# Optimization experiments

Hardware: AMD Instinct MI355X
Metric: run time of the kernel (lower is better)

Reference implementation:

```python
import jax, jax.numpy as jnp
import numpy as np

N_LAYERS = 2
D_MODEL = 768
D_INNER = 1536
D_STATE = 16
D_CONV = 4
DT_RANK = 48
VOCAB = 50257
EPS = 1e-5


def _rms(x, w):
    return x * jax.lax.rsqrt(jnp.mean(x * x, axis=-1, keepdims=True) + EPS) * w


def _mixer(x, in_w, cw, cb, xp_w, dt_w, dt_b, a_log, d_skip, out_w):
    b, l, _ = x.shape
    xz = x @ in_w.T                                  # (b,l,2*d_in)
    u, z = jnp.split(xz, 2, axis=-1)                 # each (b,l,d_in)
    # causal depthwise conv1d
    uc = jax.lax.conv_general_dilated(
        u.transpose(0, 2, 1), cw[:, None, :], (1,), [(D_CONV - 1, 0)],
        feature_group_count=D_INNER, dimension_numbers=("NCH", "OIH", "NCH"))
    u = jax.nn.silu((uc + cb[:, None]).transpose(0, 2, 1))
    x_dbl = u @ xp_w.T                               # (b,l,dt_rank+2n)
    dt, B, C = jnp.split(x_dbl, [DT_RANK, DT_RANK + D_STATE], axis=-1)
    delta = jax.nn.softplus(dt @ dt_w.T + dt_b)      # (b,l,d_in)
    A = -jnp.exp(a_log)                              # (d_in,n)
    dA = jnp.exp(delta[..., None] * A)               # (b,l,d_in,n)
    dBu = delta[..., None] * B[:, :, None, :] * u[..., None]

    def step(h, inp):
        dA_t, dBu_t, C_t = inp
        h = dA_t * h + dBu_t
        return h, jnp.einsum("bdn,bn->bd", h, C_t)

    h0 = jnp.zeros((b, D_INNER, D_STATE), x.dtype)
    _, ys = jax.lax.scan(step, h0, (dA.transpose(1, 0, 2, 3),
                                    dBu.transpose(1, 0, 2, 3),
                                    C.transpose(1, 0, 2)))
    y = ys.transpose(1, 0, 2) + u * d_skip           # (b,l,d_in)
    y = y * jax.nn.silu(z)
    return y @ out_w.T


def setup_inputs() -> dict:
    key = jax.random.key(0)
    ks = jax.random.split(key, 12)
    std = 0.02
    emb = jax.random.normal(ks[0], (VOCAB, D_MODEL), jnp.float32) * std
    emb = emb.at[0].set(0.0)  # padding_idx=0
    tokens = jax.random.randint(ks[1], (2, 1024), 0, VOCAB)
    a_log = jnp.tile(jnp.log(jnp.arange(1, D_STATE + 1, dtype=jnp.float32)),
                     (N_LAYERS, D_INNER, 1))
    return {
        "tokens": tokens,
        "emb": emb,
        "norm_w": jnp.ones((N_LAYERS, D_MODEL), jnp.float32),
        "in_proj_w": jax.random.normal(ks[2], (N_LAYERS, 2 * D_INNER, D_MODEL), jnp.float32) * std,
        "conv_w": jax.random.normal(ks[3], (N_LAYERS, D_INNER, D_CONV), jnp.float32) * 0.1,
        "conv_b": jnp.zeros((N_LAYERS, D_INNER), jnp.float32),
        "x_proj_w": jax.random.normal(ks[4], (N_LAYERS, DT_RANK + 2 * D_STATE, D_INNER), jnp.float32) * std,
        "dt_proj_w": jax.random.normal(ks[5], (N_LAYERS, D_INNER, DT_RANK), jnp.float32) * (DT_RANK ** -0.5),
        "dt_proj_b": jax.random.uniform(ks[6], (N_LAYERS, D_INNER), jnp.float32, -4.6, -2.0),
        "A_log": a_log,
        "D": jnp.ones((N_LAYERS, D_INNER), jnp.float32),
        "out_proj_w": jax.random.normal(ks[7], (N_LAYERS, D_MODEL, D_INNER), jnp.float32) * (std / np.sqrt(2 * N_LAYERS)),
        "normf_w": jnp.ones((D_MODEL,), jnp.float32),
        "lm_head_w": jax.random.normal(ks[8], (VOCAB, D_MODEL), jnp.float32) * std,
    }


def reference(tokens, emb, norm_w, in_proj_w, conv_w, conv_b, x_proj_w,
              dt_proj_w, dt_proj_b, A_log, D, out_proj_w, normf_w, lm_head_w):
    x = emb[tokens]                                  # (b,l,d_model)
    for i in range(N_LAYERS):
        x = x + _mixer(_rms(x, norm_w[i]), in_proj_w[i], conv_w[i], conv_b[i],
                       x_proj_w[i], dt_proj_w[i], dt_proj_b[i], A_log[i],
                       D[i], out_proj_w[i])
    x = _rms(x, normf_w)
    return x @ lm_head_w.T                           # (b,l,vocab)
```

## Files before the change

### kernel.cpp

```cpp
#include <hip/hip_runtime.h>
#include <hip/hip_bf16.h>
#include <math.h>

#define DM 768
#define DI 1536
#define DSN 16
#define NB 2
#define SL 1024
#define MROWS 2048
#define VOC 50257
#define VOCP 50304
#define EPSR 1e-5f

typedef __attribute__((ext_vector_type(8))) short short8;
typedef __attribute__((ext_vector_type(4))) float f32x4;
typedef __attribute__((ext_vector_type(4))) unsigned short us4;
typedef unsigned short u16;

__device__ inline u16 f2bf(float f) {
    unsigned u = __builtin_bit_cast(unsigned, f);
    u += 0x7FFFu + ((u >> 16) & 1u);
    return (u16)(u >> 16);
}

__global__ void k_embed(const int* __restrict__ tok, const float* __restrict__ emb,
                        float* __restrict__ x) {
    int r = blockIdx.x;
    int t = tok[r];
    const float* src = emb + (size_t)t * DM;
    float* dst = x + (size_t)r * DM;
    for (int i = threadIdx.x; i < DM; i += 256) dst[i] = src[i];
}

__global__ __launch_bounds__(256)
void k_rmsnorm_bf16(const float* __restrict__ x, const float* __restrict__ w,
                    u16* __restrict__ out) {
    int r = blockIdx.x;
    const float* row = x + (size_t)r * DM;
    int c0 = threadIdx.x * 3;
    float v[3]; float ss = 0.f;
#pragma unroll
    for (int i = 0; i < 3; ++i) { v[i] = row[c0 + i]; ss += v[i] * v[i]; }
#pragma unroll
    for (int o = 32; o > 0; o >>= 1) ss += __shfl_down(ss, o);
    __shared__ float s[4];
    int lane = threadIdx.x & 63, wv = threadIdx.x >> 6;
    if (lane == 0) s[wv] = ss;
    __syncthreads();
    float sc = rsqrtf((s[0] + s[1] + s[2] + s[3]) / (float)DM + EPSR);
#pragma unroll
    for (int i = 0; i < 3; ++i)
        out[(size_t)r * DM + c0 + i] = f2bf(v[i] * sc * w[c0 + i]);
}

__global__ void k_cvt_pad4(const float* __restrict__ src, u16* __restrict__ dst,
                           int sr, int sc, int sld, int dc, long total4) {
    long i4 = (long)blockIdx.x * 256 + threadIdx.x;
    if (i4 >= total4) return;
    long i = i4 * 4;
    int r = (int)(i / dc), c0 = (int)(i % dc);
    us4 o;
#pragma unroll
    for (int e = 0; e < 4; ++e) {
        int c = c0 + e;
        float v = (r < sr && c < sc) ? src[(size_t)r * sld + c] : 0.f;
        o[e] = f2bf(v);
    }
    *(us4*)&dst[i] = o;
}

__global__ void k_conv_silu(const float* __restrict__ xz, const float* __restrict__ cw,
                            const float* __restrict__ cb, float* __restrict__ uc,
                            u16* __restrict__ ucb) {
    int d = blockIdx.x * 256 + threadIdx.x;
    int r = blockIdx.y;
    int l = r & (SL - 1);
    float acc = cb[d];
#pragma unroll
    for (int j = 0; j < 4; ++j) {
        int ls = l - 3 + j;
        if (ls >= 0) acc += xz[(size_t)(r - 3 + j) * (2 * DI) + d] * cw[d * 4 + j];
    }
    float s = acc / (1.f + __expf(-acc));
    uc[(size_t)r * DI + d] = s;
    ucb[(size_t)r * DI + d] = f2bf(s);
}

__global__ void k_softplus(const float* __restrict__ in, const float* __restrict__ b,
                           float* __restrict__ out) {
    int i = blockIdx.x * 256 + threadIdx.x;
    int d = i % DI;
    float v = in[i] + b[d];
    out[i] = (v > 20.f) ? v : log1pf(__expf(v));
}

__global__ __launch_bounds__(512)
void k_scan2(const float* __restrict__ delta, const float* __restrict__ uc,
             const float* __restrict__ xdbl, const float* __restrict__ xz,
             const float* __restrict__ alog, const float* __restrict__ Dp,
             u16* __restrict__ ybf) {
    __shared__ float ds2[8][16][20], us2[8][16][20], bn2[8][16][20], cn2[8][16][20];
    __shared__ float Sm[8][16][16], Pm[8][16][16];
    int b  = blockIdx.x / 96;
    int d0 = (blockIdx.x % 96) * 16;
    int tid = threadIdx.x, w = tid >> 6, lane = tid & 63;
    int ch = lane >> 2, nq = lane & 3;
    int d = d0 + ch;
    float A[4];
#pragma unroll
    for (int k = 0; k < 4; ++k) A[k] = -__expf(alog[d * DSN + nq + 4 * k]);
    int tb = w * 128;

    float h[4] = {0.f, 0.f, 0.f, 0.f};
    float sdl = 0.f;
    for (int t0 = 0; t0 < 128; t0 += 16) {
        int row0 = b * SL + tb + t0;
#pragma unroll
        for (int i = 0; i < 4; ++i) {
            int lin = i * 64 + lane, tt = lin >> 4, cc = lin & 15;
            size_t row = (size_t)(row0 + tt);
            ds2[w][cc][tt] = delta[row * DI + d0 + cc];
            us2[w][cc][tt] = uc[row * DI + d0 + cc];
            bn2[w][cc][tt] = xdbl[row * 128 + 48 + cc];
        }
#pragma unroll
        for (int g4 = 0; g4 < 4; ++g4) {
            f32x4 dl = *(const f32x4*)&ds2[w][ch][g4 * 4];
            f32x4 uv = *(const f32x4*)&us2[w][ch][g4 * 4];
            f32x4 bv[4];
#pragma unroll
            for (int k = 0; k < 4; ++k) bv[k] = *(const f32x4*)&bn2[w][nq + 4 * k][g4 * 4];
#pragma unroll
            for (int s = 0; s < 4; ++s) {
                float du = dl[s] * uv[s];
                sdl += dl[s];
#pragma unroll
                for (int k = 0; k < 4; ++k) {
                    float dA = __expf(dl[s] * A[k]);
                    h[k] = h[k] * dA + du * bv[k][s];
                }
            }
        }
    }
#pragma unroll
    for (int k = 0; k < 4; ++k) {
        Sm[w][ch][nq + 4 * k] = h[k];
        Pm[w][ch][nq + 4 * k] = __expf(A[k] * sdl);
    }
    __syncthreads();
    if (tid < 256) {
        int c2 = tid >> 4, n2 = tid & 15;
        float H = 0.f;
#pragma unroll
        for (int g = 0; g < 8; ++g) {
            float hi = H;
            H = Pm[g][c2][n2] * H + Sm[g][c2][n2];
            Sm[g][c2][n2] = hi;
        }
    }
    __syncthreads();
    float Dv = Dp[d];
#pragma unroll
    for (int k = 0; k < 4; ++k) h[k] = Sm[w][ch][nq + 4 * k];
    for (int t0 = 0; t0 < 128; t0 += 16) {
        int row0 = b * SL + tb + t0;
#pragma unroll
        for (int i = 0; i < 4; ++i) {
            int lin = i * 64 + lane, tt = lin >> 4, cc = lin & 15;
            size_t row = (size_t)(row0 + tt);
            ds2[w][cc][tt] = delta[row * DI + d0 + cc];
            us2[w][cc][tt] = uc[row * DI + d0 + cc];
            bn2[w][cc][tt] = xdbl[row * 128 + 48 + cc];
            cn2[w][cc][tt] = xdbl[row * 128 + 64 + cc];
        }
#pragma unroll
        for (int g4 = 0; g4 < 4; ++g4) {
            f32x4 dl = *(const f32x4*)&ds2[w][ch][g4 * 4];
            f32x4 uv = *(const f32x4*)&us2[w][ch][g4 * 4];
            f32x4 bv[4], cv[4];
#pragma unroll
            for (int k = 0; k < 4; ++k) {
                bv[k] = *(const f32x4*)&bn2[w][nq + 4 * k][g4 * 4];
                cv[k] = *(const f32x4*)&cn2[w][nq + 4 * k][g4 * 4];
            }
#pragma unroll
            for (int s = 0; s < 4; ++s) {
                float du = dl[s] * uv[s];
                float p = 0.f;
#pragma unroll
                for (int k = 0; k < 4; ++k) {
                    float dA = __expf(dl[s] * A[k]);
                    h[k] = h[k] * dA + du * bv[k][s];
                    p += h[k] * cv[k][s];
                }
                p += __shfl_xor(p, 1);
                p += __shfl_xor(p, 2);
                if (nq == 0) {
                    size_t row = (size_t)(row0 + g4 * 4 + s);
                    float z = xz[row * (2 * DI) + DI + d];
                    float y = p + uv[s] * Dv;
                    y *= z / (1.f + __expf(-z));
                    ybf[row * DI + d] = f2bf(y);
                }
            }
        }
    }
}

template <bool ADD_RES, bool NGUARD>
__global__ __launch_bounds__(256)
void k_gemm_bt(const u16* __restrict__ A, const u16* __restrict__ W,
               float* __restrict__ C, const float* __restrict__ RES,
               int K, int ldc, int nmax, int nTm) {
    __shared__ u16 Al[128 * 32];
    __shared__ u16 Wl[128 * 32];
    int nwg = gridDim.x;
    int qc = nwg >> 3, rc = nwg & 7;
    int xcd = blockIdx.x & 7, j = blockIdx.x >> 3;
    int wg = (xcd < rc ? xcd * (qc + 1) : rc * (qc + 1) + (xcd - rc) * qc) + j;
    int m0 = (wg % nTm) * 128, n0 = (wg / nTm) * 128;

    int tid = threadIdx.x, wave = tid >> 6, lane = tid & 63;
    int wm = wave >> 1, wn = wave & 1;
    f32x4 acc[4][4] = {};
    const int rS = (lane >> 2);
    const int kS = (((lane & 3) ^ ((lane >> 3) & 3)) * 8);
    const int kofs = (((lane >> 4) ^ ((lane >> 1) & 3)) * 8);
    const int fr = lane & 15;

    for (int k0 = 0; k0 < K; k0 += 32) {
#pragma unroll
        for (int i = 0; i < 2; ++i) {
            int rowA = m0 + wave * 32 + i * 16 + rS;
            const u16* ga = A + (size_t)rowA * K + k0 + kS;
            __builtin_amdgcn_global_load_lds(
                (const __attribute__((address_space(1))) void*)ga,
                (__attribute__((address_space(3))) void*)(&Al[wave * 1024 + i * 512]),
                16, 0, 0);
            int rowW = n0 + wave * 32 + i * 16 + rS;
            const u16* gw = W + (size_t)rowW * K + k0 + kS;
            __builtin_amdgcn_global_load_lds(
                (const __attribute__((address_space(1))) void*)gw,
                (__attribute__((address_space(3))) void*)(&Wl[wave * 1024 + i * 512]),
                16, 0, 0);
        }
        __syncthreads();
        short8 af[4], bfr[4];
#pragma unroll
        for (int f = 0; f < 4; ++f) {
            af[f]  = *(const short8*)&Al[(wm * 64 + f * 16 + fr) * 32 + kofs];
            bfr[f] = *(const short8*)&Wl[(wn * 64 + f * 16 + fr) * 32 + kofs];
        }
#pragma unroll
        for (int i = 0; i < 4; ++i)
#pragma unroll
            for (int jj = 0; jj < 4; ++jj)
                acc[i][jj] = __builtin_amdgcn_mfma_f32_16x16x32_bf16(af[i], bfr[jj], acc[i][jj], 0, 0, 0);
        __syncthreads();
    }
    int r4 = (lane >> 4) * 4;
#pragma unroll
    for (int i = 0; i < 4; ++i)
#pragma unroll
        for (int jj = 0; jj < 4; ++jj) {
            int col = n0 + wn * 64 + jj * 16 + fr;
            if (NGUARD && col >= nmax) continue;
#pragma unroll
            for (int rr = 0; rr < 4; ++rr) {
                int row = m0 + wm * 64 + i * 16 + r4 + rr;
                size_t off = (size_t)row * ldc + col;
                float v = acc[i][jj][rr];
                if (ADD_RES) v += RES[off];
                C[off] = v;
            }
        }
}

extern "C" void kernel_launch(void* const* d_in, const int* in_sizes, int n_in,
                              void* d_out, int out_size, void* d_ws, size_t ws_size,
                              hipStream_t stream) {
    (void)in_sizes; (void)n_in; (void)out_size;
    const int*   tok   = (const int*)d_in[0];
    const float* emb   = (const float*)d_in[1];
    const float* normw = (const float*)d_in[2];
    const float* inw   = (const float*)d_in[3];
    const float* cw    = (const float*)d_in[4];
    const float* cb    = (const float*)d_in[5];
    const float* xpw   = (const float*)d_in[6];
    const float* dtw   = (const float*)d_in[7];
    const float* dtb   = (const float*)d_in[8];
    const float* alog  = (const float*)d_in[9];
    const float* Dp    = (const float*)d_in[10];
    const float* outw  = (const float*)d_in[11];
    const float* normf = (const float*)d_in[12];
    const float* lmw   = (const float*)d_in[13];
    float* out = (float*)d_out;

    char* p = (char*)d_ws;
    auto alloc = [&](size_t bytes) { char* r = p; p += (bytes + 255) & ~(size_t)255; return r; };
    float* x     = (float*)alloc((size_t)MROWS * DM * 4);
    u16*   xnb   = (u16*)  alloc((size_t)MROWS * DM * 2);
    float* xz    = (float*)alloc((size_t)MROWS * 2 * DI * 4);
    float* uc    = (float*)alloc((size_t)MROWS * DI * 4);
    u16*   ucb   = (u16*)  alloc((size_t)MROWS * DI * 2);
    float* xdbl  = (float*)alloc((size_t)MROWS * 128 * 4);
    u16*   xdblb = (u16*)  alloc((size_t)MROWS * 64 * 2);
    float* dtraw = (float*)alloc((size_t)MROWS * DI * 4);
    float* delta = (float*)alloc((size_t)MROWS * DI * 4);
    u16*   ybf   = (u16*)  alloc((size_t)MROWS * DI * 2);
    u16*   winb  = (u16*)  alloc((size_t)(2 * DI) * DM * 2);
    u16*   wxpb  = (u16*)  alloc((size_t)128 * DI * 2);
    u16*   wdtb  = (u16*)  alloc((size_t)DI * 64 * 2);
    u16*   woutb = (u16*)  alloc((size_t)DM * DI * 2);
    u16*   wlmb  = (u16*)  alloc((size_t)VOCP * DM * 2);
    if ((size_t)(p - (char*)d_ws) > ws_size) return;

    {
        long t4 = (long)VOCP * DM / 4;
        k_cvt_pad4<<<dim3((unsigned)((t4 + 255) / 256)), 256, 0, stream>>>(
            lmw, wlmb, VOC, DM, DM, DM, t4);
    }

    k_embed<<<MROWS, 256, 0, stream>>>(tok, emb, x);

    for (int i = 0; i < NB; ++i) {
        k_rmsnorm_bf16<<<MROWS, 256, 0, stream>>>(x, normw + i * DM, xnb);

        { long t4 = (long)(2 * DI) * DM / 4;
          k_cvt_pad4<<<dim3((unsigned)((t4 + 255) / 256)), 256, 0, stream>>>(
              inw + (size_t)i * 2 * DI * DM, winb, 2 * DI, DM, DM, DM, t4); }
        k_gemm_bt<false, false><<<dim3(16 * (2 * DI / 128)), 256, 0, stream>>>(
            xnb, winb, xz, nullptr, DM, 2 * DI, 2 * DI, 16);

        k_conv_silu<<<dim3(DI / 256, MROWS), 256, 0, stream>>>(
            xz, cw + (size_t)i * DI * 4, cb + (size_t)i * DI, uc, ucb);

        { long t4 = (long)128 * DI / 4;
          k_cvt_pad4<<<dim3((unsigned)((t4 + 255) / 256)), 256, 0, stream>>>(
              xpw + (size_t)i * 80 * DI, wxpb, 80, DI, DI, DI, t4); }
        k_gemm_bt<false, false><<<dim3(16 * 1), 256, 0, stream>>>(
            ucb, wxpb, xdbl, nullptr, DI, 128, 128, 16);

        { long t4 = (long)MROWS * 64 / 4;
          k_cvt_pad4<<<dim3((unsigned)((t4 + 255) / 256)), 256, 0, stream>>>(
              xdbl, xdblb, MROWS, 64, 128, 64, t4); }
        { long t4 = (long)DI * 64 / 4;
          k_cvt_pad4<<<dim3((unsigned)((t4 + 255) / 256)), 256, 0, stream>>>(
              dtw + (size_t)i * DI * 48, wdtb, DI, 48, 48, 64, t4); }
        k_gemm_bt<false, false><<<dim3(16 * (DI / 128)), 256, 0, stream>>>(
            xdblb, wdtb, dtraw, nullptr, 64, DI, DI, 16);

        k_softplus<<<dim3(MROWS * DI / 256), 256, 0, stream>>>(dtraw, dtb + i * DI, delta);

        k_scan2<<<dim3(NB * (DI / 16)), 512, 0, stream>>>(
            delta, uc, xdbl, xz, alog + (size_t)i * DI * DSN, Dp + i * DI, ybf);

        { long t4 = (long)DM * DI / 4;
          k_cvt_pad4<<<dim3((unsigned)((t4 + 255) / 256)), 256, 0, stream>>>(
              outw + (size_t)i * DM * DI, woutb, DM, DI, DI, DI, t4); }
        k_gemm_bt<true, false><<<dim3(16 * (DM / 128)), 256, 0, stream>>>(
            ybf, woutb, x, x, DI, DM, DM, 16);
    }

    k_rmsnorm_bf16<<<MROWS, 256, 0, stream>>>(x, normf, xnb);
    k_gemm_bt<false, true><<<dim3(16 * (VOCP / 128)), 256, 0, stream>>>(
        xnb, wlmb, out, nullptr, DM, VOC, VOC, 16);
}
```

Measured before the change: 837.9 us.

## Add 256x256 pipelined MFMA GEMM with direct LDS loads for LM head

Replaces the 128-tile GEMM for the vocab projection with a new 256x256-tile, 512-thread kernel. It uses global_load_lds direct-to-LDS staging with swizzled addressing, double-buffered half-tile prefetch interleaved with MFMA blocks, setprio, and an XCD-aware block remap. Vocab padding is increased to a multiple of 256. The goal is more data reuse per tile and better latency hiding for the dominant LM-head GEMM, at the cost of heavy manual scheduling, many barriers and high register pressure.

```diff
diff --git a/kernel.cpp b/kernel.cpp
--- a/kernel.cpp
+++ b/kernel.cpp
@@ -9,7 +9,7 @@
 #define SL 1024
 #define MROWS 2048
 #define VOC 50257
-#define VOCP 50304
+#define VOCP 50432
 #define EPSR 1e-5f
 
 typedef __attribute__((ext_vector_type(8))) short short8;
@@ -273,6 +273,134 @@
                 if (ADD_RES) v += RES[off];
                 C[off] = v;
             }
+        }
+}
+
+#define G_LDS16(g, l) __builtin_amdgcn_global_load_lds( \
+    (const __attribute__((address_space(1))) void*)(g), \
+    (__attribute__((address_space(3))) void*)(l), 16, 0, 0)
+#define BAR  __builtin_amdgcn_s_barrier()
+#define LGK0 do { asm volatile("s_waitcnt lgkmcnt(0)" ::: "memory"); \
+                  __builtin_amdgcn_sched_barrier(0); } while (0)
+#define VMC6 asm volatile("s_waitcnt vmcnt(6)" ::: "memory")
+#define VMC0 asm volatile("s_waitcnt vmcnt(0)" ::: "memory")
+
+#define STAGE_HT(t, op, half, GB, RB) do {                                   \
+    const u16* _g = (GB) + (size_t)((RB) + (half) * 128 + (w << 3) + srow) * K \
+                    + (t) * 64 + scol;                                        \
+    G_LDS16(_g, &lds[(t) & 1][op][half][w << 9]);                             \
+    G_LDS16(_g + (size_t)64 * K, &lds[(t) & 1][op][half][4096 + (w << 9)]);   \
+} while (0)
+
+#define RD_A(dst, t, mq) do {                                                \
+    _Pragma("unroll") for (int _m = 0; _m < 4; ++_m)                          \
+    _Pragma("unroll") for (int _k = 0; _k < 2; ++_k)                          \
+        dst[_m][_k] = *(const short8*)&lds[(t) & 1][0][wm]                    \
+            [(mq) * 4096 + _m * 1024 + _k * 32 + rd_off];                     \
+} while (0)
+
+#define RD_B(t, nq) do {                                                     \
+    _Pragma("unroll") for (int _n = 0; _n < 2; ++_n)                          \
+    _Pragma("unroll") for (int _k = 0; _k < 2; ++_k)                          \
+        bfv[_n][_k] = *(const short8*)&lds[(t) & 1][1][wbh]                   \
+            [wbr * 4096 + (nq) * 2048 + _n * 1024 + _k * 32 + rd_off];        \
+} while (0)
+
+#define MM16(AF, mq, nq) do {                                                \
+    __builtin_amdgcn_s_setprio(1);                                           \
+    _Pragma("unroll") for (int _m = 0; _m < 4; ++_m)                          \
+    _Pragma("unroll") for (int _n = 0; _n < 2; ++_n)                          \
+    _Pragma("unroll") for (int _k = 0; _k < 2; ++_k)                          \
+        acc[(mq) * 4 + _m][(nq) * 2 + _n] =                                   \
+            __builtin_amdgcn_mfma_f32_16x16x32_bf16(                          \
+                AF[_m][_k], bfv[_n][_k], acc[(mq) * 4 + _m][(nq) * 2 + _n],   \
+                0, 0, 0);                                                     \
+    __builtin_amdgcn_s_setprio(0);                                           \
+} while (0)
+
+template <int K>
+__global__ __launch_bounds__(512, 2)
+void k_gemm256(const u16* __restrict__ Ap, const u16* __restrict__ Wp,
+               float* __restrict__ C, int ldc, int nmax, int nTm) {
+    constexpr int NT = K / 64;
+    constexpr int NI = NT / 2;
+    __shared__ __align__(16) u16 lds[2][2][2][8192];
+
+    int per8 = gridDim.x >> 3;
+    int wg = (blockIdx.x & 7) * per8 + (blockIdx.x >> 3);
+    int m0 = (wg % nTm) * 256, n0 = (wg / nTm) * 256;
+
+    int tid = threadIdx.x, w = tid >> 6, lane = tid & 63;
+    int wm = w >> 2, wn = w & 3, wbh = wn >> 1, wbr = wn & 1;
+    int fr = lane & 15;
+    int rd_off = fr * 64 + (((lane >> 4) * 8) ^ (((fr >> 2) & 1) * 16));
+    int srow = lane >> 3;
+    int scol = ((lane & 7) * 8) ^ (((lane >> 5) & 1) * 16);
+
+    f32x4 acc[8][4] = {};
+    short8 af0[4][2], af1[4][2], bfv[2][2];
+
+    STAGE_HT(0, 0, 0, Ap, m0); STAGE_HT(0, 0, 1, Ap, m0);
+    STAGE_HT(0, 1, 0, Wp, n0); STAGE_HT(0, 1, 1, Wp, n0);
+    STAGE_HT(1, 0, 0, Ap, m0); STAGE_HT(1, 0, 1, Ap, m0);
+    STAGE_HT(1, 1, 0, Wp, n0);
+    VMC6; BAR;
+
+    for (int i = 0; i < NI - 1; ++i) {
+        const int ta = 2 * i, tb = 2 * i + 1;
+        RD_A(af0, ta, 0); RD_B(ta, 0);
+        STAGE_HT(tb, 1, 1, Wp, n0);
+        BAR; LGK0; MM16(af0, 0, 0); BAR;
+        RD_A(af1, ta, 1);
+        STAGE_HT(ta + 2, 0, 0, Ap, m0);
+        BAR; LGK0; MM16(af1, 1, 0); BAR;
+        RD_B(ta, 1);
+        STAGE_HT(ta + 2, 0, 1, Ap, m0);
+        BAR; LGK0; MM16(af1, 1, 1); BAR;
+        STAGE_HT(ta + 2, 1, 0, Wp, n0);
+        BAR; MM16(af0, 0, 1); VMC6; BAR;
+        RD_A(af0, tb, 0); RD_B(tb, 0);
+        STAGE_HT(ta + 2, 1, 1, Wp, n0);
+        BAR; LGK0; MM16(af0, 0, 0); BAR;
+        RD_A(af1, tb, 1);
+        STAGE_HT(ta + 3, 0, 0, Ap, m0);
+        BAR; LGK0; MM16(af1, 1, 0); BAR;
+        RD_B(tb, 1);
+        STAGE_HT(ta + 3, 0, 1, Ap, m0);
+        BAR; LGK0; MM16(af1, 1, 1); BAR;
+        STAGE_HT(ta + 3, 1, 0, Wp, n0);
+        BAR; MM16(af0, 0, 1); VMC6; BAR;
+    }
+    {
+        const int ta = NT - 2, tb = NT - 1;
+        RD_A(af0, ta, 0); RD_B(ta, 0);
+        STAGE_HT(tb, 1, 1, Wp, n0);
+        BAR; LGK0; MM16(af0, 0, 0); BAR;
+        RD_A(af1, ta, 1);
+        BAR; LGK0; MM16(af1, 1, 0); BAR;
+        RD_B(ta, 1);
+        BAR; LGK0; MM16(af1, 1, 1); BAR;
+        BAR; MM16(af0, 0, 1); VMC0; BAR;
+        RD_A(af0, tb, 0); RD_B(tb, 0);
+        BAR; LGK0; MM16(af0, 0, 0); BAR;
+        RD_A(af1, tb, 1);
+        BAR; LGK0; MM16(af1, 1, 0); BAR;
+        RD_B(tb, 1);
+        BAR; LGK0; MM16(af1, 1, 1); BAR;
+        BAR; MM16(af0, 0, 1); BAR;
+    }
+
+    int r4 = (lane >> 4) * 4;
+#pragma unroll
+    for (int mi = 0; mi < 8; ++mi)
+#pragma unroll
+        for (int ni = 0; ni < 4; ++ni) {
+            int col = n0 + wn * 64 + (ni >> 1) * 32 + (ni & 1) * 16 + fr;
+            if (col >= nmax) continue;
+            int row = m0 + wm * 128 + (mi >> 2) * 64 + (mi & 3) * 16 + r4;
+#pragma unroll
+            for (int rr = 0; rr < 4; ++rr)
+                C[(size_t)(row + rr) * ldc + col] = acc[mi][ni][rr];
         }
 }
 
@@ -363,6 +491,6 @@
     }
 
     k_rmsnorm_bf16<<<MROWS, 256, 0, stream>>>(x, normf, xnb);
-    k_gemm_bt<false, true><<<dim3(16 * (VOCP / 128)), 256, 0, stream>>>(
-        xnb, wlmb, out, nullptr, DM, VOC, VOC, 16);
-}
+    k_gemm256<DM><<<dim3(8 * (VOCP / 256)), 512, 0, stream>>>(
+        xnb, wlmb, out, VOC, VOC, 8);
+}
```

Result: faster. 770.6 us (-8.0%).
